# Kernel tuning notes

Hardware: AMD Instinct MI355X
Metric: run time of the kernel (lower is better)

The kernel has to match this reference:

```python
import jax, jax.numpy as jnp
import numpy as np

N_STRUCTURES = 1000   # S
ATOMS_PER_STRUCTURE = 100  # A -> dense (structure, atom) segment grid
N_SAMPLES = 100000
N_GRAD_SAMPLES = 500000
D_FEAT = 128


def setup_inputs() -> dict:
    key = jax.random.key(0)
    k1, k2, k3, k4, k5 = jax.random.split(key, 5)
    values = jax.random.normal(k1, (N_SAMPLES, D_FEAT), dtype=jnp.float32)
    structure_ids = jnp.sort(
        jax.random.randint(k2, (N_SAMPLES,), 0, N_STRUCTURES, dtype=jnp.int32))
    gradient_data = jax.random.normal(k3, (N_GRAD_SAMPLES, 3, D_FEAT), dtype=jnp.float32)
    grad_structure = jax.random.randint(k4, (N_GRAD_SAMPLES,), 0, N_STRUCTURES, dtype=jnp.int32)
    grad_atom = jax.random.randint(k5, (N_GRAD_SAMPLES,), 0, ATOMS_PER_STRUCTURE, dtype=jnp.int32)
    return {
        "values": values,
        "structure_ids": structure_ids,
        "gradient_data": gradient_data,
        "grad_structure": grad_structure,
        "grad_atom": grad_atom,
    }


def reference(values, structure_ids, gradient_data, grad_structure, grad_atom):
    # Per-structure sum of feature rows: new_values[s] = sum_{i: structure_ids[i]==s} values[i]
    new_values = jax.ops.segment_sum(values, structure_ids, num_segments=N_STRUCTURES)
    # Positions-gradient rows are accumulated per (structure, atom) pair.
    # Dense segment id = structure * A + atom (fixed layout, same summation math
    # as the original's per-structure unique-atom compaction).
    seg_ids = grad_structure * ATOMS_PER_STRUCTURE + grad_atom
    new_gradient_data = jax.ops.segment_sum(
        gradient_data, seg_ids, num_segments=N_STRUCTURES * ATOMS_PER_STRUCTURE)
    return new_values, new_gradient_data
```

## Files before the change

kernel.cpp:

```cpp
#include <hip/hip_runtime.h>

#define N_STRUCT   1000
#define ATOMS      100
#define NSEG       (N_STRUCT * ATOMS)
#define N_SAMP     100000
#define N_GRAD     500000
#define D_FEAT     128
#define GD         (3 * D_FEAT)
#define VAL_OUT    (N_STRUCT * D_FEAT)
#define CAP        64

__global__ __launch_bounds__(D_FEAT) void values_sum_zero_kernel(
        const float* __restrict__ values, const int* __restrict__ sid,
        float* __restrict__ out, int* __restrict__ counts) {
    int s = blockIdx.x;
    int t = threadIdx.x;

    int z = s * D_FEAT + t;
    if (z < NSEG) counts[z] = 0;

    __shared__ int bounds[2];
    if (t < 2) {
        int target = s + t;
        int lo = 0, hi = N_SAMP;
        while (lo < hi) {
            int mid = (lo + hi) >> 1;
            if (sid[mid] < target) lo = mid + 1; else hi = mid;
        }
        bounds[t] = lo;
    }
    __syncthreads();
    float acc = 0.0f;
    int i = bounds[0], e = bounds[1];
    #pragma unroll 4
    for (; i < e; ++i)
        acc += values[(size_t)i * D_FEAT + t];
    out[(size_t)s * D_FEAT + t] = acc;
}

__global__ void scatter_kernel(const int* __restrict__ gs, const int* __restrict__ ga,
                               int* __restrict__ counts, int* __restrict__ rowidx) {
    int i = blockIdx.x * 256 + threadIdx.x;
    if (i < N_GRAD) {
        int seg = gs[i] * ATOMS + ga[i];
        int pos = atomicAdd(&counts[seg], 1);
        if (pos < CAP) rowidx[seg * CAP + pos] = i;
    }
}

__global__ __launch_bounds__(GD) void grad_sum_kernel(
        const float* __restrict__ grad, const int* __restrict__ counts,
        const int* __restrict__ rowidx, float* __restrict__ out) {
    int s = blockIdx.x;
    int t = threadIdx.x;
    int cnt = counts[s];
    cnt = __builtin_amdgcn_readfirstlane(cnt);
    if (cnt > CAP) cnt = CAP;
    const int* ri = rowidx + (size_t)s * CAP;

    float acc = 0.0f;
    int j = 0;
    for (; j + 4 <= cnt; j += 4) {
        int4 r4 = *reinterpret_cast<const int4*>(ri + j);
        float v0 = grad[(size_t)r4.x * GD + t];
        float v1 = grad[(size_t)r4.y * GD + t];
        float v2 = grad[(size_t)r4.z * GD + t];
        float v3 = grad[(size_t)r4.w * GD + t];
        acc += (v0 + v1) + (v2 + v3);
    }
    for (; j < cnt; ++j)
        acc += grad[(size_t)ri[j] * GD + t];
    out[(size_t)s * GD + t] = acc;
}


extern "C" void kernel_launch(void* const* d_in, const int* in_sizes, int n_in,
                              void* d_out, int out_size, void* d_ws, size_t ws_size,
                              hipStream_t stream) {
    const float* values = (const float*)d_in[0];
    const int*   sid    = (const int*)  d_in[1];
    const float* grad   = (const float*)d_in[2];
    const int*   gs     = (const int*)  d_in[3];
    const int*   ga     = (const int*)  d_in[4];
    float* out = (float*)d_out;

    int* counts = (int*)d_ws;
    int* rowidx = counts + NSEG;

    values_sum_zero_kernel<<<N_STRUCT, D_FEAT, 0, stream>>>(values, sid, out, counts);
    scatter_kernel<<<(N_GRAD + 255) / 256, 256, 0, stream>>>(gs, ga, counts, rowidx);
    grad_sum_kernel<<<NSEG, GD, 0, stream>>>(grad, counts, rowidx, out + VAL_OUT);
}
```

Before: 1.124 ms.

## Merge values sum into scatter launch and batch four segments per grad block

Counter zeroing moves into its own small kernel. The per-structure values reduction now runs in the same launch as the index scatter, two structures per 256-thread block, so the two independent pieces of work overlap. The gather-sum kernel now handles four segments per block, interleaving their row loads so more independent loads are in flight. The cost is an extra launch, plus branchier code with predicated tail loads in the gather kernel.

Result: slower. 1.213 ms (+8.0%).

```diff
diff --git a/kernel.cpp b/kernel.cpp
--- a/kernel.cpp
+++ b/kernel.cpp
@@ -10,67 +10,116 @@
 #define VAL_OUT    (N_STRUCT * D_FEAT)
 #define CAP        64
 
-__global__ __launch_bounds__(D_FEAT) void values_sum_zero_kernel(
+#define SCAT_BLOCKS ((N_GRAD + 255) / 256)
+#define VAL_BLOCKS  (N_STRUCT / 2)
+
+__global__ void zero_counts_kernel(int* __restrict__ counts) {
+    int i = blockIdx.x * 256 + threadIdx.x;
+    if (i < NSEG) counts[i] = 0;
+}
+
+__global__ __launch_bounds__(256) void scatter_values_kernel(
+        const int* __restrict__ gs, const int* __restrict__ ga,
+        int* __restrict__ counts, int* __restrict__ rowidx,
         const float* __restrict__ values, const int* __restrict__ sid,
-        float* __restrict__ out, int* __restrict__ counts) {
-    int s = blockIdx.x;
-    int t = threadIdx.x;
-
-    int z = s * D_FEAT + t;
-    if (z < NSEG) counts[z] = 0;
-
-    __shared__ int bounds[2];
-    if (t < 2) {
-        int target = s + t;
+        float* __restrict__ out) {
+    int b = blockIdx.x;
+    if (b < SCAT_BLOCKS) {
+        int i = b * 256 + threadIdx.x;
+        if (i < N_GRAD) {
+            int seg = gs[i] * ATOMS + ga[i];
+            int pos = atomicAdd(&counts[seg], 1);
+            if (pos < CAP) rowidx[seg * CAP + pos] = i;
+        }
+        return;
+    }
+    int t    = threadIdx.x;
+    int half = t >> 7;
+    int tt   = t & 127;
+    int s    = (b - SCAT_BLOCKS) * 2 + half;
+    __shared__ int bounds[2][2];
+    if (tt < 2) {
+        int target = s + tt;
         int lo = 0, hi = N_SAMP;
         while (lo < hi) {
             int mid = (lo + hi) >> 1;
             if (sid[mid] < target) lo = mid + 1; else hi = mid;
         }
-        bounds[t] = lo;
+        bounds[half][tt] = lo;
     }
     __syncthreads();
-    float acc = 0.0f;
-    int i = bounds[0], e = bounds[1];
-    #pragma unroll 4
-    for (; i < e; ++i)
-        acc += values[(size_t)i * D_FEAT + t];
-    out[(size_t)s * D_FEAT + t] = acc;
-}
-
-__global__ void scatter_kernel(const int* __restrict__ gs, const int* __restrict__ ga,
-                               int* __restrict__ counts, int* __restrict__ rowidx) {
-    int i = blockIdx.x * 256 + threadIdx.x;
-    if (i < N_GRAD) {
-        int seg = gs[i] * ATOMS + ga[i];
-        int pos = atomicAdd(&counts[seg], 1);
-        if (pos < CAP) rowidx[seg * CAP + pos] = i;
+    int lo = bounds[half][0], hi = bounds[half][1];
+    float a0 = 0.f, a1 = 0.f, a2 = 0.f, a3 = 0.f;
+    int i = lo;
+    for (; i + 4 <= hi; i += 4) {
+        a0 += values[(size_t)(i + 0) * D_FEAT + tt];
+        a1 += values[(size_t)(i + 1) * D_FEAT + tt];
+        a2 += values[(size_t)(i + 2) * D_FEAT + tt];
+        a3 += values[(size_t)(i + 3) * D_FEAT + tt];
     }
+    for (; i < hi; ++i) a0 += values[(size_t)i * D_FEAT + tt];
+    out[(size_t)s * D_FEAT + tt] = (a0 + a1) + (a2 + a3);
 }
 
 __global__ __launch_bounds__(GD) void grad_sum_kernel(
         const float* __restrict__ grad, const int* __restrict__ counts,
         const int* __restrict__ rowidx, float* __restrict__ out) {
-    int s = blockIdx.x;
-    int t = threadIdx.x;
-    int cnt = counts[s];
-    cnt = __builtin_amdgcn_readfirstlane(cnt);
-    if (cnt > CAP) cnt = CAP;
-    const int* ri = rowidx + (size_t)s * CAP;
+    int s0 = blockIdx.x * 4;
+    int t  = threadIdx.x;
+    int4 c4 = *reinterpret_cast<const int4*>(counts + s0);
+    int cnt0 = __builtin_amdgcn_readfirstlane(c4.x);
+    int cnt1 = __builtin_amdgcn_readfirstlane(c4.y);
+    int cnt2 = __builtin_amdgcn_readfirstlane(c4.z);
+    int cnt3 = __builtin_amdgcn_readfirstlane(c4.w);
+    if (cnt0 > CAP) cnt0 = CAP;
+    if (cnt1 > CAP) cnt1 = CAP;
+    if (cnt2 > CAP) cnt2 = CAP;
+    if (cnt3 > CAP) cnt3 = CAP;
+    const int* ri0 = rowidx + (size_t)(s0 + 0) * CAP;
+    const int* ri1 = rowidx + (size_t)(s0 + 1) * CAP;
+    const int* ri2 = rowidx + (size_t)(s0 + 2) * CAP;
+    const int* ri3 = rowidx + (size_t)(s0 + 3) * CAP;
 
-    float acc = 0.0f;
-    int j = 0;
-    for (; j + 4 <= cnt; j += 4) {
-        int4 r4 = *reinterpret_cast<const int4*>(ri + j);
-        float v0 = grad[(size_t)r4.x * GD + t];
-        float v1 = grad[(size_t)r4.y * GD + t];
-        float v2 = grad[(size_t)r4.z * GD + t];
-        float v3 = grad[(size_t)r4.w * GD + t];
-        acc += (v0 + v1) + (v2 + v3);
+    float acc0 = 0.f, acc1 = 0.f, acc2 = 0.f, acc3 = 0.f;
+    int m = max(max(cnt0, cnt1), max(cnt2, cnt3));
+    for (int j = 0; j < m; j += 4) {
+        if (j < cnt0) {
+            int4 r = *reinterpret_cast<const int4*>(ri0 + j);
+            int lim = cnt0 - j;
+            acc0 += grad[(size_t)r.x * GD + t];
+            if (lim > 1) acc0 += grad[(size_t)r.y * GD + t];
+            if (lim > 2) acc0 += grad[(size_t)r.z * GD + t];
+            if (lim > 3) acc0 += grad[(size_t)r.w * GD + t];
+        }
+        if (j < cnt1) {
+            int4 r = *reinterpret_cast<const int4*>(ri1 + j);
+            int lim = cnt1 - j;
+            acc1 += grad[(size_t)r.x * GD + t];
+            if (lim > 1) acc1 += grad[(size_t)r.y * GD + t];
+            if (lim > 2) acc1 += grad[(size_t)r.z * GD + t];
+            if (lim > 3) acc1 += grad[(size_t)r.w * GD + t];
+        }
+        if (j < cnt2) {
+            int4 r = *reinterpret_cast<const int4*>(ri2 + j);
+            int lim = cnt2 - j;
+            acc2 += grad[(size_t)r.x * GD + t];
+            if (lim > 1) acc2 += grad[(size_t)r.y * GD + t];
+            if (lim > 2) acc2 += grad[(size_t)r.z * GD + t];
+            if (lim > 3) acc2 += grad[(size_t)r.w * GD + t];
+        }
+        if (j < cnt3) {
+            int4 r = *reinterpret_cast<const int4*>(ri3 + j);
+            int lim = cnt3 - j;
+            acc3 += grad[(size_t)r.x * GD + t];
+            if (lim > 1) acc3 += grad[(size_t)r.y * GD + t];
+            if (lim > 2) acc3 += grad[(size_t)r.z * GD + t];
+            if (lim > 3) acc3 += grad[(size_t)r.w * GD + t];
+        }
     }
-    for (; j < cnt; ++j)
-        acc += grad[(size_t)ri[j] * GD + t];
-    out[(size_t)s * GD + t] = acc;
+    out[(size_t)(s0 + 0) * GD + t] = acc0;
+    out[(size_t)(s0 + 1) * GD + t] = acc1;
+    out[(size_t)(s0 + 2) * GD + t] = acc2;
+    out[(size_t)(s0 + 3) * GD + t] = acc3;
 }
 
 
@@ -87,7 +136,8 @@
     int* counts = (int*)d_ws;
     int* rowidx = counts + NSEG;
 
-    values_sum_zero_kernel<<<N_STRUCT, D_FEAT, 0, stream>>>(values, sid, out, counts);
-    scatter_kernel<<<(N_GRAD + 255) / 256, 256, 0, stream>>>(gs, ga, counts, rowidx);
-    grad_sum_kernel<<<NSEG, GD, 0, stream>>>(grad, counts, rowidx, out + VAL_OUT);
+    zero_counts_kernel<<<(NSEG + 255) / 256, 256, 0, stream>>>(counts);
+    scatter_values_kernel<<<SCAT_BLOCKS + VAL_BLOCKS, 256, 0, stream>>>(
+        gs, ga, counts, rowidx, values, sid, out);
+    grad_sum_kernel<<<NSEG / 4, GD, 0, stream>>>(grad, counts, rowidx, out + VAL_OUT);
 }
```

## Gather grad rows as float4 with four row-slices per block and reduce in LDS

Applied to the files above, without the earlier changes.

The gradient segment-sum kernel now has each 384-thread block handle eight segments in turn. The threads split into four groups of 96, each group loading a different gathered row as float4 and accumulating it. Partial sums are combined through shared memory and written out as float4. The aim is wider memory transactions, more independent row loads in flight per segment, and fewer tiny blocks. In exchange it adds two block barriers per segment, and the grouped loop always reads rowidx entries even for invalid slots, masking them with a zero weight.

Result: no change. 1.131 ms (+0.7%).

```diff
diff --git a/kernel.cpp b/kernel.cpp
--- a/kernel.cpp
+++ b/kernel.cpp
@@ -9,6 +9,7 @@
 #define GD         (3 * D_FEAT)
 #define VAL_OUT    (N_STRUCT * D_FEAT)
 #define CAP        64
+#define SPB        8
 
 __global__ __launch_bounds__(D_FEAT) void values_sum_zero_kernel(
         const float* __restrict__ values, const int* __restrict__ sid,
@@ -48,29 +49,53 @@
     }
 }
 
-__global__ __launch_bounds__(GD) void grad_sum_kernel(
+__global__ __launch_bounds__(384) void grad_sum_kernel(
         const float* __restrict__ grad, const int* __restrict__ counts,
         const int* __restrict__ rowidx, float* __restrict__ out) {
-    int s = blockIdx.x;
     int t = threadIdx.x;
-    int cnt = counts[s];
-    cnt = __builtin_amdgcn_readfirstlane(cnt);
-    if (cnt > CAP) cnt = CAP;
-    const int* ri = rowidx + (size_t)s * CAP;
+    int q = t / 96;
+    int c = t - q * 96;
+    __shared__ float4 red[384];
 
-    float acc = 0.0f;
-    int j = 0;
-    for (; j + 4 <= cnt; j += 4) {
-        int4 r4 = *reinterpret_cast<const int4*>(ri + j);
-        float v0 = grad[(size_t)r4.x * GD + t];
-        float v1 = grad[(size_t)r4.y * GD + t];
-        float v2 = grad[(size_t)r4.z * GD + t];
-        float v3 = grad[(size_t)r4.w * GD + t];
-        acc += (v0 + v1) + (v2 + v3);
+    int s = blockIdx.x * SPB;
+    for (int k = 0; k < SPB; ++k, ++s) {
+        int cnt = counts[s];
+        if (cnt > CAP) cnt = CAP;
+        const int* ri = rowidx + (size_t)s * CAP;
+
+        float4 acc = make_float4(0.f, 0.f, 0.f, 0.f);
+        int nb = (cnt + 3) >> 2;
+        for (int b = 0; b < nb; ++b) {
+            int j = b * 4 + q;
+            int rq = ri[j];
+            bool valid = j < cnt;
+            rq = valid ? rq : 0;
+            float w = valid ? 1.0f : 0.0f;
+            const float4* src = reinterpret_cast<const float4*>(
+                grad + (size_t)rq * GD) + c;
+            float4 v = *src;
+            acc.x = fmaf(w, v.x, acc.x);
+            acc.y = fmaf(w, v.y, acc.y);
+            acc.z = fmaf(w, v.z, acc.z);
+            acc.w = fmaf(w, v.w, acc.w);
+        }
+
+        red[t] = acc;
+        __syncthreads();
+        if (q == 0) {
+            float4 r0 = red[c];
+            float4 r1 = red[96 + c];
+            float4 r2 = red[192 + c];
+            float4 r3 = red[288 + c];
+            float4 sum;
+            sum.x = (r0.x + r1.x) + (r2.x + r3.x);
+            sum.y = (r0.y + r1.y) + (r2.y + r3.y);
+            sum.z = (r0.z + r1.z) + (r2.z + r3.z);
+            sum.w = (r0.w + r1.w) + (r2.w + r3.w);
+            *reinterpret_cast<float4*>(out + (size_t)s * GD + c * 4) = sum;
+        }
+        __syncthreads();
     }
-    for (; j < cnt; ++j)
-        acc += grad[(size_t)ri[j] * GD + t];
-    out[(size_t)s * GD + t] = acc;
 }
 
 
@@ -89,5 +114,5 @@
 
     values_sum_zero_kernel<<<N_STRUCT, D_FEAT, 0, stream>>>(values, sid, out, counts);
     scatter_kernel<<<(N_GRAD + 255) / 256, 256, 0, stream>>>(gs, ga, counts, rowidx);
-    grad_sum_kernel<<<NSEG, GD, 0, stream>>>(grad, counts, rowidx, out + VAL_OUT);
+    grad_sum_kernel<<<NSEG / SPB, 384, 0, stream>>>(grad, counts, rowidx, out + VAL_OUT);
 }
```
